# Performance work log

Hardware: AMD Instinct MI355X
Metric: run time of the kernel (lower is better)

The kernel has to match this reference:

```python
import jax, jax.numpy as jnp
import numpy as np
import math

D_MODEL = 512
N_HEADS = 8
HEAD_DIM = D_MODEL // N_HEADS


def setup_inputs() -> dict:
    key = jax.random.key(0)
    k1, k2, k3 = jax.random.split(key, 3)
    B, T = 2, 4096
    x = jax.random.normal(k1, (B, T, D_MODEL), dtype=jnp.float32)
    # nn.Linear weights: stored as [out, in], applied as x @ W.T
    W_QKV = jax.random.normal(k2, (3 * D_MODEL, D_MODEL), dtype=jnp.float32) * (1.0 / math.sqrt(D_MODEL))
    W_O = jax.random.normal(k3, (D_MODEL, D_MODEL), dtype=jnp.float32) * (1.0 / math.sqrt(D_MODEL))
    return {"x": x, "W_QKV": W_QKV, "W_O": W_O}


def reference(x, W_QKV, W_O):
    B, T, C = x.shape
    qkv = (x @ W_QKV.T).reshape(B, T, 3, N_HEADS, HEAD_DIM)
    q, k, v = qkv[:, :, 0], qkv[:, :, 1], qkv[:, :, 2]  # [B,T,H,D]
    # scores: [B,H,T,T]
    scale = math.sqrt(HEAD_DIM)
    attn = jnp.einsum('bqhd,bkhd->bhqk', q, k) / scale
    causal_mask = jnp.triu(jnp.ones((T, T), dtype=bool), k=1)
    attn = jnp.where(causal_mask, -jnp.inf, attn)
    attn = jax.nn.softmax(attn, axis=-1)
    out = jnp.einsum('bhqk,bkhd->bqhd', attn, v).reshape(B, T, C)
    return out @ W_O.T
```

## Files before the change

### kernel.cpp

```cpp
#include <hip/hip_runtime.h>
#include <hip/hip_bf16.h>

typedef __bf16 bf16_t;
typedef __bf16 bf16x8 __attribute__((ext_vector_type(8)));
typedef __bf16 bf16x4 __attribute__((ext_vector_type(4)));
typedef float  floatx4 __attribute__((ext_vector_type(4)));

static __device__ __forceinline__ floatx4 mfma16(bf16x8 a, bf16x8 b, floatx4 c) {
  return __builtin_amdgcn_mfma_f32_16x16x32_bf16(a, b, c, 0, 0, 0);
}

typedef __attribute__((address_space(3))) void lds_vp;
typedef __attribute__((address_space(1))) void glb_vp;
#define GLDS16(g, l) \
  __builtin_amdgcn_global_load_lds((glb_vp*)(g), (lds_vp*)(l), 16, 0, 0)

__global__ void cvt_all_kernel(const float* __restrict__ x,
                               const float* __restrict__ wqkv,
                               const float* __restrict__ wo,
                               bf16_t* __restrict__ xb,
                               bf16_t* __restrict__ wqkvb,
                               bf16_t* __restrict__ wob) {
  int i = blockIdx.x * blockDim.x + threadIdx.x;
  const float4* src; bf16x4* dst; int off;
  if (i < 1048576)      { src = (const float4*)x;    dst = (bf16x4*)xb;    off = i; }
  else if (i < 1245184) { src = (const float4*)wqkv; dst = (bf16x4*)wqkvb; off = i - 1048576; }
  else                  { src = (const float4*)wo;   dst = (bf16x4*)wob;   off = i - 1245184; }
  float4 v = src[off];
  bf16x4 o;
  o[0] = (bf16_t)v.x; o[1] = (bf16_t)v.y; o[2] = (bf16_t)v.z; o[3] = (bf16_t)v.w;
  dst[off] = o;
}

__global__ __launch_bounds__(256) void gemm_qkv(
    const bf16_t* __restrict__ A, const bf16_t* __restrict__ B,
    bf16_t* __restrict__ Qo, bf16_t* __restrict__ Ko, bf16_t* __restrict__ Vto)
{
  __shared__ __align__(16) bf16_t As[2][128 * 64];
  __shared__ __align__(16) bf16_t Bs[2][128 * 64];
  const int tid  = threadIdx.x;
  const int lane = tid & 63;
  const int w    = tid >> 6;
  const int quad = lane >> 4;
  const int l15  = lane & 15;
  const int l7   = lane & 7;
  const int wm   = w & 1;
  const int wn   = w >> 1;
  const int K    = 512;

  floatx4 acc[4][4];
  #pragma unroll
  for (int i = 0; i < 4; ++i)
    #pragma unroll
    for (int j = 0; j < 4; ++j)
      acc[i][j] = (floatx4){0.f, 0.f, 0.f, 0.f};

  const bf16_t* Ab = A + (size_t)blockIdx.x * 128 * K;
  const bf16_t* Bb = B + (size_t)blockIdx.y * 128 * K;

  auto stage = [&](int buf, int k0) {
    #pragma unroll
    for (int i = 0; i < 4; ++i) {
      int c = tid + 256 * i;
      int row = c >> 3, colc = c & 7;
      int gofs = ((colc ^ (row & 7)) << 3);
      GLDS16(&Ab[(size_t)row * K + k0 + gofs], &As[buf][c * 8]);
      GLDS16(&Bb[(size_t)row * K + k0 + gofs], &Bs[buf][c * 8]);
    }
  };

  stage(0, 0);
  for (int it = 0; it < 8; ++it) {
    const int cur = it & 1;
    __syncthreads();
    if (it + 1 < 8) stage(cur ^ 1, (it + 1) << 6);
    #pragma unroll
    for (int ks = 0; ks < 2; ++ks) {
      bf16x8 af[4], bfr[4];
      #pragma unroll
      for (int t = 0; t < 4; ++t) {
        af[t]  = *(const bf16x8*)&As[cur][(wm * 64 + t * 16 + l15) * 64 +
                                         (((ks * 4 + quad) ^ l7) << 3)];
        bfr[t] = *(const bf16x8*)&Bs[cur][(wn * 64 + t * 16 + l15) * 64 +
                                         (((ks * 4 + quad) ^ l7) << 3)];
      }
      #pragma unroll
      for (int mt = 0; mt < 4; ++mt)
        #pragma unroll
        for (int nt = 0; nt < 4; ++nt)
          acc[mt][nt] = mfma16(af[mt], bfr[nt], acc[mt][nt]);
    }
  }

  if (blockIdx.y < 8) {
    #pragma unroll
    for (int mt = 0; mt < 4; ++mt) {
      #pragma unroll
      for (int nt = 0; nt < 4; ++nt) {
        #pragma unroll
        for (int r = 0; r < 4; ++r) {
          int m = blockIdx.x * 128 + wm * 64 + mt * 16 + quad * 4 + r;
          int n = blockIdx.y * 128 + wn * 64 + nt * 16 + l15;
          float v = acc[mt][nt][r];
          int b = m >> 12, t = m & 4095;
          int h = (n >> 6) & 7, d = n & 63;
          size_t bh = (size_t)(b * 8 + h);
          if (n < 512)
            Qo[bh * 262144 + (size_t)t * 64 + d] = (bf16_t)(v * 0.18033688f);
          else
            Ko[bh * 262144 + (size_t)t * 64 + d] = (bf16_t)v;
        }
      }
    }
  } else {
    __syncthreads();
    bf16_t* L = &As[0][0];
    #pragma unroll
    for (int mt = 0; mt < 4; ++mt)
      #pragma unroll
      for (int nt = 0; nt < 4; ++nt) {
        int n_l = wn * 64 + nt * 16 + l15;
        int mc  = wm * 8 + mt * 2 + (quad >> 1);
        bf16x4 v4;
        #pragma unroll
        for (int r = 0; r < 4; ++r) v4[r] = (bf16_t)acc[mt][nt][r];
        *(bf16x4*)&L[n_l * 128 + ((mc ^ (n_l & 15)) << 3) + (quad & 1) * 4] = v4;
      }
    __syncthreads();
    const int t0 = (blockIdx.x & 31) * 128;
    const int b  = blockIdx.x >> 5;
    #pragma unroll
    for (int i = 0; i < 8; ++i) {
      int c = tid + 256 * i;
      int n_l = c >> 4, tc = c & 15;
      int h = ((blockIdx.y - 8) << 1) | (n_l >> 6);
      int d = n_l & 63;
      size_t bh = (size_t)(b * 8 + h);
      int base0 = (tc >> 2) * 32 + (tc & 3) * 4;
      bf16x4 lo = *(const bf16x4*)&L[n_l * 128 +
                     (((base0 >> 3) ^ (n_l & 15)) << 3) + (base0 & 7)];
      bf16x4 hi = *(const bf16x4*)&L[n_l * 128 +
                     ((((base0 + 16) >> 3) ^ (n_l & 15)) << 3) + (base0 & 7)];
      bf16x8 o;
      #pragma unroll
      for (int e = 0; e < 4; ++e) { o[e] = lo[e]; o[e + 4] = hi[e]; }
      *(bf16x8*)&Vto[bh * 262144 + (size_t)d * 4096 + t0 + tc * 8] = o;
    }
  }
}

__global__ __launch_bounds__(256) void gemm_out(
    const bf16_t* __restrict__ A, const bf16_t* __restrict__ B,
    float* __restrict__ Cf)
{
  __shared__ __align__(16) bf16_t As[2][64 * 64];
  __shared__ __align__(16) bf16_t Bs[2][128 * 64];
  const int tid  = threadIdx.x;
  const int lane = tid & 63;
  const int w    = tid >> 6;
  const int quad = lane >> 4;
  const int l15  = lane & 15;
  const int l7   = lane & 7;

  floatx4 acc[4][2];
  #pragma unroll
  for (int i = 0; i < 4; ++i)
    #pragma unroll
    for (int j = 0; j < 2; ++j)
      acc[i][j] = (floatx4){0.f, 0.f, 0.f, 0.f};

  const bf16_t* Ab = A + (size_t)blockIdx.x * 64 * 512;
  const bf16_t* Bb = B + (size_t)blockIdx.y * 128 * 512;

  auto stage = [&](int buf, int k0) {
    #pragma unroll
    for (int i = 0; i < 2; ++i) {
      int c = tid + 256 * i;
      int row = c >> 3, colc = c & 7;
      GLDS16(&Ab[(size_t)row * 512 + k0 + ((colc ^ (row & 7)) << 3)],
             &As[buf][c * 8]);
    }
    #pragma unroll
    for (int i = 0; i < 4; ++i) {
      int c = tid + 256 * i;
      int row = c >> 3, colc = c & 7;
      GLDS16(&Bb[(size_t)row * 512 + k0 + ((colc ^ (row & 7)) << 3)],
             &Bs[buf][c * 8]);
    }
  };

  stage(0, 0);
  for (int it = 0; it < 8; ++it) {
    const int cur = it & 1;
    __syncthreads();
    if (it + 1 < 8) stage(cur ^ 1, (it + 1) << 6);
    #pragma unroll
    for (int ks = 0; ks < 2; ++ks) {
      bf16x8 af[4], bfr[2];
      #pragma unroll
      for (int t = 0; t < 4; ++t)
        af[t]  = *(const bf16x8*)&As[cur][(t * 16 + l15) * 64 +
                                         (((ks * 4 + quad) ^ l7) << 3)];
      #pragma unroll
      for (int t = 0; t < 2; ++t)
        bfr[t] = *(const bf16x8*)&Bs[cur][(w * 32 + t * 16 + l15) * 64 +
                                         (((ks * 4 + quad) ^ l7) << 3)];
      #pragma unroll
      for (int mt = 0; mt < 4; ++mt)
        #pragma unroll
        for (int nt = 0; nt < 2; ++nt)
          acc[mt][nt] = mfma16(af[mt], bfr[nt], acc[mt][nt]);
    }
  }

  #pragma unroll
  for (int mt = 0; mt < 4; ++mt)
    #pragma unroll
    for (int nt = 0; nt < 2; ++nt)
      #pragma unroll
      for (int r = 0; r < 4; ++r) {
        int m = blockIdx.x * 64 + mt * 16 + quad * 4 + r;
        int n = blockIdx.y * 128 + w * 32 + nt * 16 + l15;
        Cf[(size_t)m * 512 + n] = acc[mt][nt][r];
      }
}

__global__ __launch_bounds__(512, 4) void attn_kernel(
    const bf16_t* __restrict__ Qg, const bf16_t* __restrict__ Kgl,
    const bf16_t* __restrict__ Vtg, bf16_t* __restrict__ Og)
{
  __shared__ __align__(16) bf16_t Ks[2][128 * 64];
  __shared__ __align__(16) bf16_t Vts[2][64 * 128];

  const int tid  = threadIdx.x;
  const int lane = tid & 63;
  const int w    = tid >> 6;
  const int grp  = w >> 2;
  const int ws   = w & 3;
  const int quad = lane >> 4;
  const int l15  = lane & 15;

  const int id = blockIdx.x + 32 * blockIdx.y;
  const int k8 = id & 7;
  const int j  = id >> 3;
  const int jj = j & 31;
  const int bh = 2 * k8 + (jj & 1);
  const int p  = jj >> 1;
  const int x    = (j < 32) ? p : 15 - p;
  const int half = (j < 32) ? 0 : 1;
  const int qtA = 31 - x, qtB = x;
  const int qt_g = grp ? qtB : qtA;
  const size_t bh_off = (size_t)bh * 262144;
  const int b = bh >> 3, h = bh & 7;

  const int gq = qt_g * 128 + half * 64 + ws * 16 + l15;
  bf16x8 aq0, aq1;
  {
    const bf16_t* Qp = Qg + bh_off + (size_t)gq * 64;
    aq0 = *(const bf16x8*)&Qp[quad * 8];
    aq1 = *(const bf16x8*)&Qp[32 + quad * 8];
  }
  bf16x8 ones;
  #pragma unroll
  for (int i = 0; i < 8; ++i) ones[i] = (bf16_t)1.0f;

  floatx4 acc_o[4], acc_l;
  #pragma unroll
  for (int dt = 0; dt < 4; ++dt) acc_o[dt] = (floatx4){0.f, 0.f, 0.f, 0.f};
  acc_l = (floatx4){0.f, 0.f, 0.f, 0.f};

  auto stage = [&](int buf, int kt) {
    const bf16_t* Kp = Kgl + bh_off + (size_t)kt * 8192;
    const bf16_t* Vp = Vtg + bh_off + (size_t)kt * 128;
    #pragma unroll
    for (int i = 0; i < 2; ++i) {
      int c = tid + 512 * i;
      int row = c >> 3, colc = c & 7;
      GLDS16(&Kp[row * 64 + ((colc ^ (row & 7)) << 3)], &Ks[buf][c * 8]);
    }
    #pragma unroll
    for (int i = 0; i < 2; ++i) {
      int c = tid + 512 * i;
      int row = c >> 4, colc = c & 15;
      GLDS16(&Vp[(size_t)row * 4096 + ((colc ^ (row & 15)) << 3)], &Vts[buf][c * 8]);
    }
  };

  stage(0, 0);
  const int nkt = qtA + 1;
  for (int kt = 0; kt < nkt; ++kt) {
    const int cur = kt & 1;
    __syncthreads();
    if (kt + 1 < nkt) stage(cur ^ 1, kt + 1);

    if (kt <= qt_g) {
      floatx4 s[8];
      #pragma unroll
      for (int nt = 0; nt < 8; ++nt) s[nt] = (floatx4){0.f, 0.f, 0.f, 0.f};
      #pragma unroll
      for (int nt = 0; nt < 8; ++nt) {
        bf16x8 bk0 = *(const bf16x8*)&Ks[cur][(nt * 16 + l15) * 64 +
                                             ((quad ^ (l15 & 7)) << 3)];
        s[nt] = mfma16(bk0, aq0, s[nt]);
      }
      #pragma unroll
      for (int nt = 0; nt < 8; ++nt) {
        bf16x8 bk1 = *(const bf16x8*)&Ks[cur][(nt * 16 + l15) * 64 +
                                             (((4 + quad) ^ (l15 & 7)) << 3)];
        s[nt] = mfma16(bk1, aq1, s[nt]);
      }

      if (kt == qt_g) {
        #pragma unroll
        for (int nt = 0; nt < 8; ++nt)
          #pragma unroll
          for (int r = 0; r < 4; ++r)
            if (kt * 128 + nt * 16 + quad * 4 + r > gq) s[nt][r] = -3.0e38f;
      }
      #pragma unroll
      for (int nt = 0; nt < 8; ++nt)
        #pragma unroll
        for (int r = 0; r < 4; ++r)
          s[nt][r] = exp2f(s[nt][r]);

      #pragma unroll
      for (int kc = 0; kc < 4; ++kc) {
        bf16x8 pb;
        #pragma unroll
        for (int r = 0; r < 4; ++r) {
          pb[r]     = (bf16_t)s[kc * 2][r];
          pb[r + 4] = (bf16_t)s[kc * 2 + 1][r];
        }
        acc_l = mfma16(ones, pb, acc_l);
        #pragma unroll
        for (int dt = 0; dt < 4; ++dt) {
          int row = dt * 16 + l15;
          bf16x8 av = *(const bf16x8*)&Vts[cur][row * 128 +
                                               (((kc * 4 + quad) ^ l15) << 3)];
          acc_o[dt] = mfma16(av, pb, acc_o[dt]);
        }
      }
    }
  }

  __syncthreads();
  bf16_t* Ot = &Ks[0][grp * 4096];
  const float rl = 1.0f / acc_l[0];
  const int t_own = ws * 16 + l15;
  #pragma unroll
  for (int dt = 0; dt < 4; ++dt) {
    bf16x4 o4;
    #pragma unroll
    for (int r = 0; r < 4; ++r) o4[r] = (bf16_t)(acc_o[dt][r] * rl);
    *(bf16x4*)&Ot[t_own * 64 +
                  (((dt * 2 + (quad >> 1)) ^ (t_own & 7)) << 3) + (quad & 1) * 4] = o4;
  }
  __syncthreads();
  const int gtid = tid & 255;
  #pragma unroll
  for (int i = 0; i < 2; ++i) {
    int cc = gtid + 256 * i;
    int t = cc >> 3, c = cc & 7;
    bf16x8 o8 = *(const bf16x8*)&Ot[t * 64 + ((c ^ (t & 7)) << 3)];
    int trow = qt_g * 128 + half * 64 + t;
    *(bf16x8*)&Og[((size_t)b * 4096 + trow) * 512 + h * 64 + c * 8] = o8;
  }
}

extern "C" void kernel_launch(void* const* d_in, const int* in_sizes, int n_in,
                              void* d_out, int out_size, void* d_ws, size_t ws_size,
                              hipStream_t stream) {
  const float* x    = (const float*)d_in[0];
  const float* wqkv = (const float*)d_in[1];
  const float* wo   = (const float*)d_in[2];
  float* out = (float*)d_out;

  char* ws = (char*)d_ws;
  bf16_t* xb    = (bf16_t*)(ws);
  bf16_t* wqkvb = (bf16_t*)(ws + 8388608);
  bf16_t* wob   = (bf16_t*)(ws + 9961472);
  bf16_t* Qb    = (bf16_t*)(ws + 10485760);
  bf16_t* Kb    = (bf16_t*)(ws + 18874368);
  bf16_t* Vtb   = (bf16_t*)(ws + 27262976);
  bf16_t* Ob    = xb;

  cvt_all_kernel<<<5120, 256, 0, stream>>>(x, wqkv, wo, xb, wqkvb, wob);

  gemm_qkv<<<dim3(64, 12), 256, 0, stream>>>(xb, wqkvb, Qb, Kb, Vtb);
  attn_kernel<<<dim3(32, 16), 512, 0, stream>>>(Qb, Kb, Vtb, Ob);
  gemm_out<<<dim3(128, 4), 256, 0, stream>>>(Ob, wob, out);
}
```

Before: 164.4 us.

## Shrink attention tiles to 64 keys per step with 256-thread blocks

The attention kernel drops its paired 128-row query-tile scheme (two 4-wave groups sharing 128-key K/V tiles, one group idling once its causal range ended) and becomes 1024 independent 256-thread blocks, each handling 64 queries against 64-key K/V tiles. Query tiles are ordered so heavy and light causal tiles interleave across the grid. The aim is to remove the idle waves and the wasted masking work at the diagonal, and to cut LDS per block for higher occupancy. In exchange, each K/V tile is reused by fewer queries and the loop runs twice as many barrier-synchronized iterations.

```diff
diff --git a/kernel.cpp b/kernel.cpp
--- a/kernel.cpp
+++ b/kernel.cpp
@@ -225,35 +225,30 @@
       }
 }
 
-__global__ __launch_bounds__(512, 4) void attn_kernel(
+__global__ __launch_bounds__(256, 4) void attn_kernel(
     const bf16_t* __restrict__ Qg, const bf16_t* __restrict__ Kgl,
     const bf16_t* __restrict__ Vtg, bf16_t* __restrict__ Og)
 {
-  __shared__ __align__(16) bf16_t Ks[2][128 * 64];
-  __shared__ __align__(16) bf16_t Vts[2][64 * 128];
+  __shared__ __align__(16) bf16_t Ks[2][64 * 64];
+  __shared__ __align__(16) bf16_t Vts[2][64 * 64];
 
   const int tid  = threadIdx.x;
   const int lane = tid & 63;
   const int w    = tid >> 6;
-  const int grp  = w >> 2;
-  const int ws   = w & 3;
   const int quad = lane >> 4;
   const int l15  = lane & 15;
 
-  const int id = blockIdx.x + 32 * blockIdx.y;
+  const int id = blockIdx.x;
   const int k8 = id & 7;
   const int j  = id >> 3;
-  const int jj = j & 31;
-  const int bh = 2 * k8 + (jj & 1);
-  const int p  = jj >> 1;
-  const int x    = (j < 32) ? p : 15 - p;
-  const int half = (j < 32) ? 0 : 1;
-  const int qtA = 31 - x, qtB = x;
-  const int qt_g = grp ? qtB : qtA;
+  const int bh = 2 * k8 + (j & 1);
+  const int jj = j >> 1;
+  const int u  = jj & 15, rr = jj >> 4;
+  const int qt = (rr == 0) ? u : (rr == 1) ? 63 - u : (rr == 2) ? 31 - u : 32 + u;
   const size_t bh_off = (size_t)bh * 262144;
   const int b = bh >> 3, h = bh & 7;
 
-  const int gq = qt_g * 128 + half * 64 + ws * 16 + l15;
+  const int gq = qt * 64 + w * 16 + l15;
   bf16x8 aq0, aq1;
   {
     const bf16_t* Qp = Qg + bh_off + (size_t)gq * 64;
@@ -270,83 +265,81 @@
   acc_l = (floatx4){0.f, 0.f, 0.f, 0.f};
 
   auto stage = [&](int buf, int kt) {
-    const bf16_t* Kp = Kgl + bh_off + (size_t)kt * 8192;
-    const bf16_t* Vp = Vtg + bh_off + (size_t)kt * 128;
+    const bf16_t* Kp = Kgl + bh_off + (size_t)kt * 4096;
+    const bf16_t* Vp = Vtg + bh_off + (size_t)kt * 64;
     #pragma unroll
     for (int i = 0; i < 2; ++i) {
-      int c = tid + 512 * i;
+      int c = tid + 256 * i;
       int row = c >> 3, colc = c & 7;
       GLDS16(&Kp[row * 64 + ((colc ^ (row & 7)) << 3)], &Ks[buf][c * 8]);
     }
     #pragma unroll
     for (int i = 0; i < 2; ++i) {
-      int c = tid + 512 * i;
-      int row = c >> 4, colc = c & 15;
-      GLDS16(&Vp[(size_t)row * 4096 + ((colc ^ (row & 15)) << 3)], &Vts[buf][c * 8]);
+      int c = tid + 256 * i;
+      int row = c >> 3, colc = c & 7;
+      GLDS16(&Vp[(size_t)row * 4096 + ((colc ^ (row & 7)) << 3)], &Vts[buf][c * 8]);
     }
   };
 
   stage(0, 0);
-  const int nkt = qtA + 1;
+  const int nkt = qt + 1;
   for (int kt = 0; kt < nkt; ++kt) {
     const int cur = kt & 1;
     __syncthreads();
     if (kt + 1 < nkt) stage(cur ^ 1, kt + 1);
 
-    if (kt <= qt_g) {
-      floatx4 s[8];
-      #pragma unroll
-      for (int nt = 0; nt < 8; ++nt) s[nt] = (floatx4){0.f, 0.f, 0.f, 0.f};
-      #pragma unroll
-      for (int nt = 0; nt < 8; ++nt) {
-        bf16x8 bk0 = *(const bf16x8*)&Ks[cur][(nt * 16 + l15) * 64 +
-                                             ((quad ^ (l15 & 7)) << 3)];
-        s[nt] = mfma16(bk0, aq0, s[nt]);
-      }
-      #pragma unroll
-      for (int nt = 0; nt < 8; ++nt) {
-        bf16x8 bk1 = *(const bf16x8*)&Ks[cur][(nt * 16 + l15) * 64 +
-                                             (((4 + quad) ^ (l15 & 7)) << 3)];
-        s[nt] = mfma16(bk1, aq1, s[nt]);
-      }
-
-      if (kt == qt_g) {
-        #pragma unroll
-        for (int nt = 0; nt < 8; ++nt)
-          #pragma unroll
-          for (int r = 0; r < 4; ++r)
-            if (kt * 128 + nt * 16 + quad * 4 + r > gq) s[nt][r] = -3.0e38f;
-      }
-      #pragma unroll
-      for (int nt = 0; nt < 8; ++nt)
+    floatx4 s[4];
+    #pragma unroll
+    for (int nt = 0; nt < 4; ++nt) s[nt] = (floatx4){0.f, 0.f, 0.f, 0.f};
+    #pragma unroll
+    for (int nt = 0; nt < 4; ++nt) {
+      bf16x8 bk0 = *(const bf16x8*)&Ks[cur][(nt * 16 + l15) * 64 +
+                                           ((quad ^ (l15 & 7)) << 3)];
+      s[nt] = mfma16(bk0, aq0, s[nt]);
+    }
+    #pragma unroll
+    for (int nt = 0; nt < 4; ++nt) {
+      bf16x8 bk1 = *(const bf16x8*)&Ks[cur][(nt * 16 + l15) * 64 +
+                                           (((4 + quad) ^ (l15 & 7)) << 3)];
+      s[nt] = mfma16(bk1, aq1, s[nt]);
+    }
+
+    if (kt == qt) {
+      #pragma unroll
+      for (int nt = 0; nt < 4; ++nt)
         #pragma unroll
         for (int r = 0; r < 4; ++r)
-          s[nt][r] = exp2f(s[nt][r]);
-
-      #pragma unroll
-      for (int kc = 0; kc < 4; ++kc) {
-        bf16x8 pb;
-        #pragma unroll
-        for (int r = 0; r < 4; ++r) {
-          pb[r]     = (bf16_t)s[kc * 2][r];
-          pb[r + 4] = (bf16_t)s[kc * 2 + 1][r];
-        }
-        acc_l = mfma16(ones, pb, acc_l);
-        #pragma unroll
-        for (int dt = 0; dt < 4; ++dt) {
-          int row = dt * 16 + l15;
-          bf16x8 av = *(const bf16x8*)&Vts[cur][row * 128 +
-                                               (((kc * 4 + quad) ^ l15) << 3)];
-          acc_o[dt] = mfma16(av, pb, acc_o[dt]);
-        }
+          if (kt * 64 + nt * 16 + quad * 4 + r > gq) s[nt][r] = -3.0e38f;
+    }
+    #pragma unroll
+    for (int nt = 0; nt < 4; ++nt)
+      #pragma unroll
+      for (int r = 0; r < 4; ++r)
+        s[nt][r] = exp2f(s[nt][r]);
+
+    #pragma unroll
+    for (int kc = 0; kc < 2; ++kc) {
+      bf16x8 pb;
+      #pragma unroll
+      for (int r = 0; r < 4; ++r) {
+        pb[r]     = (bf16_t)s[kc * 2][r];
+        pb[r + 4] = (bf16_t)s[kc * 2 + 1][r];
+      }
+      acc_l = mfma16(ones, pb, acc_l);
+      #pragma unroll
+      for (int dt = 0; dt < 4; ++dt) {
+        int row = dt * 16 + l15;
+        bf16x8 av = *(const bf16x8*)&Vts[cur][row * 64 +
+                                             (((kc * 4 + quad) ^ (l15 & 7)) << 3)];
+        acc_o[dt] = mfma16(av, pb, acc_o[dt]);
       }
     }
   }
 
   __syncthreads();
-  bf16_t* Ot = &Ks[0][grp * 4096];
+  bf16_t* Ot = &Ks[0][0];
   const float rl = 1.0f / acc_l[0];
-  const int t_own = ws * 16 + l15;
+  const int t_own = w * 16 + l15;
   #pragma unroll
   for (int dt = 0; dt < 4; ++dt) {
     bf16x4 o4;
@@ -356,13 +349,12 @@
                   (((dt * 2 + (quad >> 1)) ^ (t_own & 7)) << 3) + (quad & 1) * 4] = o4;
   }
   __syncthreads();
-  const int gtid = tid & 255;
   #pragma unroll
   for (int i = 0; i < 2; ++i) {
-    int cc = gtid + 256 * i;
+    int cc = tid + 256 * i;
     int t = cc >> 3, c = cc & 7;
     bf16x8 o8 = *(const bf16x8*)&Ot[t * 64 + ((c ^ (t & 7)) << 3)];
-    int trow = qt_g * 128 + half * 64 + t;
+    int trow = qt * 64 + t;
     *(bf16x8*)&Og[((size_t)b * 4096 + trow) * 512 + h * 64 + c * 8] = o8;
   }
 }
@@ -387,6 +379,6 @@
   cvt_all_kernel<<<5120, 256, 0, stream>>>(x, wqkv, wo, xb, wqkvb, wob);
 
   gemm_qkv<<<dim3(64, 12), 256, 0, stream>>>(xb, wqkvb, Qb, Kb, Vtb);
-  attn_kernel<<<dim3(32, 16), 512, 0, stream>>>(Qb, Kb, Vtb, Ob);
+  attn_kernel<<<1024, 256, 0, stream>>>(Qb, Kb, Vtb, Ob);
   gemm_out<<<dim3(128, 4), 256, 0, stream>>>(Ob, wob, out);
 }
```

Result: slower. 172.4 us (+4.9%).
